# Optimization experiments

Measured on AMD Instinct MI355X. Metric: run time of the kernel, lower is better.

The kernel has to match this reference:

```python
import jax, jax.numpy as jnp
import numpy as np

EMBED = 512
HEADS = 64
DK = EMBED // HEADS  # == n_wires_attn == 8
NW_FFN = 8
FFN = 2048
EPS = 1e-5


def _layernorm(x, g, b):
    mu = jnp.mean(x, axis=-1, keepdims=True)
    var = jnp.var(x, axis=-1, keepdims=True)
    return (x - mu) * jax.lax.rsqrt(var + EPS) * g + b


def setup_inputs() -> dict:
    key = jax.random.key(0)
    ks = jax.random.split(key, 12)
    d = {
        "x": jax.random.normal(ks[0], (4, 1024, EMBED), dtype=jnp.float32),
        # attention quantum RX params (one per wire, shared across heads/tokens)
        "phi": jax.random.normal(ks[1], (DK,), dtype=jnp.float32) * 0.1,
        # combine_heads linear
        "Wc": jax.random.normal(ks[2], (EMBED, EMBED), dtype=jnp.float32) / np.sqrt(EMBED),
        "bc": jnp.zeros((EMBED,), dtype=jnp.float32),
        # FFN quantum RY params
        "theta": jax.random.normal(ks[3], (NW_FFN,), dtype=jnp.float32) * 0.1,
        "W1": jax.random.normal(ks[4], (NW_FFN, FFN), dtype=jnp.float32) / np.sqrt(NW_FFN),
        "b1": jnp.zeros((FFN,), dtype=jnp.float32),
        "W2": jax.random.normal(ks[5], (FFN, EMBED), dtype=jnp.float32) / np.sqrt(FFN),
        "b2": jnp.zeros((EMBED,), dtype=jnp.float32),
        "g1": jnp.ones((EMBED,), dtype=jnp.float32),
        "be1": jnp.zeros((EMBED,), dtype=jnp.float32),
        "g2": jnp.ones((EMBED,), dtype=jnp.float32),
        "be2": jnp.zeros((EMBED,), dtype=jnp.float32),
    }
    return d


def reference(x, phi, Wc, bc, theta, W1, b1, W2, b2, g1, be1, g2, be2):
    B, S, E = x.shape
    # --- quantum attention projections ---
    # Per head-row of DK features: RX(x_i) encoder then trainable RX(phi_i),
    xh = x.reshape(B, S, HEADS, DK)
    qkv = jnp.cos(xh + phi)                     # [B,S,H,DK]
    qkv = jnp.transpose(qkv, (0, 2, 1, 3))      # [B,H,S,DK]
    scores = jnp.einsum('bhqd,bhkd->bhqk', qkv, qkv) / jnp.sqrt(jnp.float32(DK))
    attn = jax.nn.softmax(scores, axis=-1)
    out = jnp.einsum('bhqk,bhkd->bhqd', attn, qkv)
    out = jnp.transpose(out, (0, 2, 1, 3)).reshape(B, S, E)
    attn_out = out @ Wc.T if False else out @ Wc + bc  # combine_heads linear
    x1 = _layernorm(x + attn_out, g1, be1)
    # --- quantum FFN: RX(x_i) then trainable RY(theta_i) -> <Z> = cos(x_i)*cos(theta_i)
    qout = jnp.cos(x1[..., :NW_FFN]) * jnp.cos(theta)   # [B,S,NW_FFN]
    h = jax.nn.relu(qout @ W1 + b1)
    ffn_out = h @ W2 + b2
    return _layernorm(x1 + ffn_out, g2, be2)
```

## Files before the change

### kernel.cpp

```cpp
#include <hip/hip_runtime.h>
#include <hip/hip_bf16.h>
#include <math.h>

#define B 4
#define S 1024
#define E 512
#define H 64
#define DK 8
#define FFN 2048
#define BS (B*S)

#define CSCALE 0.7141879f

#if __has_builtin(__builtin_amdgcn_exp2f)
#define EXP2F(x) __builtin_amdgcn_exp2f(x)
#else
#define EXP2F(x) exp2f(x)
#endif

typedef __attribute__((ext_vector_type(8))) short short8;
typedef __attribute__((ext_vector_type(4))) float float4a;

union U8 { short8 v; unsigned u[4]; };
union F4 { float4a v; float f[4]; };

__device__ __forceinline__ unsigned short f2bf(float f) {
    unsigned u = __builtin_bit_cast(unsigned, f);
    u = (u + 0x7fffu + ((u >> 16) & 1u)) >> 16;
    return (unsigned short)u;
}
__device__ __forceinline__ float bf2f(unsigned short h) {
    return __builtin_bit_cast(float, (unsigned)h << 16);
}
__device__ __forceinline__ unsigned packbf(float a, float b) {
    return __builtin_amdgcn_perm(__builtin_bit_cast(unsigned, a),
                                 __builtin_bit_cast(unsigned, b), 0x07060302u);
}
__device__ __forceinline__ unsigned packbf_rn(float a, float b) {
    return ((unsigned)f2bf(a) << 16) | f2bf(b);
}
__device__ __forceinline__ int pidx(int k) {
    return (k & ~31) | (((k >> 2) & 3) << 3) | (((k >> 4) & 1) << 2) | (k & 3);
}

__global__ __launch_bounds__(512) void attn_conv_kernel(const float* __restrict__ x,
                                                        const float* __restrict__ phi,
                                                        const float* __restrict__ Wc,
                                                        const float* __restrict__ W2,
                                                        const float* __restrict__ W1,
                                                        const float* __restrict__ b1,
                                                        unsigned short* __restrict__ Afrag,
                                                        unsigned short* __restrict__ W2f,
                                                        unsigned short* __restrict__ Wcf,
                                                        unsigned short* __restrict__ W1f) {
    __shared__ unsigned short kv[(S + 16) * DK];
    __shared__ unsigned short vtp[9][S + 8];
    int bid = blockIdx.x;
    int tid = threadIdx.x;

    if (bid >= 512) {
        int idx = (bid - 512) * 512 + tid;
        if (idx < 131072) {
            int lane = idx & 63, c = idx >> 6;
            int ntile = c >> 6, kb32 = c & 63;
            int g = lane >> 4, col = lane & 15;
            int n = ntile * 16 + col, kb = kb32 * 32;
            short8 o;
            #pragma unroll
            for (int j = 0; j < 8; j++) {
                int k = kb + 16 * (j >> 2) + 4 * g + (j & 3);
                o[j] = (short)f2bf(W2[(size_t)k * 512 + n]);
            }
            *(short8*)&W2f[(size_t)idx * 8] = o;
        } else if (idx < 163840) {
            int i2 = idx - 131072;
            int lane = i2 & 63, c = i2 >> 6;
            int ntile = c >> 4, kb32 = c & 15;
            int g = lane >> 4, col = lane & 15;
            int n = ntile * 16 + col, kb = kb32 * 32;
            short8 o;
            #pragma unroll
            for (int j = 0; j < 8; j++)
                o[j] = (short)f2bf(Wc[(size_t)(kb + g * 8 + j) * 512 + n]);
            *(short8*)&Wcf[(size_t)i2 * 8] = o;
        } else {
            int i3 = idx - 163840;
            int lane = i3 & 63, c = i3 >> 6;
            int g = lane >> 4, col = lane & 15;
            int f = (c >> 1) * 32 + (c & 1) * 16 + col;
            short8 o = {0,0,0,0,0,0,0,0};
            if (g == 0) {
                #pragma unroll
                for (int j = 0; j < 8; j++) o[j] = (short)f2bf(W1[j * FFN + f]);
            } else if (g == 1) {
                o[0] = (short)f2bf(b1[f]);
            }
            *(short8*)&W1f[(size_t)i3 * 8] = o;
        }
        return;
    }

    int head = bid >> 1, qhalf = bid & 1;
    int b = head >> 6, hh = head & 63;

    float ph[DK];
    #pragma unroll
    for (int d = 0; d < DK; d++) ph[d] = phi[d];

    const short8 z8 = {0,0,0,0,0,0,0,0};
    for (int r = tid; r < S; r += 512) {
        const float* xp = x + ((size_t)(b * S + r)) * E + hh * DK;
        float4 u = *(const float4*)xp;
        float4 v = *(const float4*)(xp + 4);
        float c[8] = {__cosf(u.x+ph[0]), __cosf(u.y+ph[1]), __cosf(u.z+ph[2]), __cosf(u.w+ph[3]),
                      __cosf(v.x+ph[4]), __cosf(v.y+ph[5]), __cosf(v.z+ph[6]), __cosf(v.w+ph[7])};
        unsigned* kp = (unsigned*)&kv[r * DK];
        #pragma unroll
        for (int d = 0; d < 4; d++)
            kp[d] = packbf_rn(c[2*d+1] * CSCALE, c[2*d] * CSCALE);
        int pr = pidx(r);
        #pragma unroll
        for (int d = 0; d < DK; d++) vtp[d][pr] = f2bf(c[d]);
        vtp[8][pr] = 0x3F80;
    }
    if (tid < 16) *(short8*)&kv[(S + tid) * DK] = z8;
    __syncthreads();

    int w = tid >> 6, lane = tid & 63, col = lane & 15, g = lane >> 4;
    bool g0 = (g == 0);
    int q0 = qhalf * 512 + w * 64;
    const float4a zc = {0.f,0.f,0.f,0.f};

    short8 aq[4];
    #pragma unroll
    for (int t = 0; t < 4; t++)
        aq[t] = g0 ? *(const short8*)&kv[(q0 + t*16 + col) * DK] : z8;

    float4a acc[4];
    #pragma unroll
    for (int t = 0; t < 4; t++) acc[t] = zc;

    int vrow = col < 8 ? col : 8;
    const unsigned short* vbase = &vtp[vrow][0];

    int off0 = g0 ? col * DK : S * DK;
    int off1 = g0 ? (16 + col) * DK : S * DK;
    int stepo = g0 ? 32 * DK : 0;

    for (int kb = 0; kb < S; kb += 32) {
        short8 bk0 = *(const short8*)&kv[off0];
        short8 bk1 = *(const short8*)&kv[off1];
        off0 += stepo; off1 += stepo;
        short8 vf = *(const short8*)(vbase + kb + g * 8);
        #pragma unroll
        for (int t = 0; t < 4; t++) {
            float4a s0 = __builtin_amdgcn_mfma_f32_16x16x32_bf16(bk0, aq[t], zc, 0,0,0);
            float4a s1 = __builtin_amdgcn_mfma_f32_16x16x32_bf16(bk1, aq[t], zc, 0,0,0);
            F4 S0, S1; S0.v = s0; S1.v = s1;
            float e00 = EXP2F(S0.f[0]);
            float e01 = EXP2F(S0.f[1]);
            float e02 = EXP2F(S0.f[2]);
            float e03 = EXP2F(S0.f[3]);
            float e10 = EXP2F(S1.f[0]);
            float e11 = EXP2F(S1.f[1]);
            float e12 = EXP2F(S1.f[2]);
            float e13 = EXP2F(S1.f[3]);
            U8 pf;
            pf.u[0] = packbf(e01, e00);
            pf.u[1] = packbf(e03, e02);
            pf.u[2] = packbf(e11, e10);
            pf.u[3] = packbf(e13, e12);
            acc[t] = __builtin_amdgcn_mfma_f32_16x16x32_bf16(vf, pf.v, acc[t], 0,0,0);
        }
    }
    int lp8 = ((hh & 3) * 16 + col) * 8;
    #pragma unroll
    for (int t = 0; t < 4; t++) {
        F4 a; a.v = acc[t];
        float denom = __shfl(a.f[0], 32 + col);
        float inv = __builtin_amdgcn_rcpf(denom);
        if (g < 2) {
            int chunk = (hh >> 2) * 256 + ((b << 6) | (qhalf << 5) | (w << 2) | t);
            uint2 o;
            o.x = packbf_rn(a.f[1] * inv, a.f[0] * inv);
            o.y = packbf_rn(a.f[3] * inv, a.f[2] * inv);
            *(uint2*)&Afrag[(size_t)chunk * 512 + lp8 + g * 4] = o;
        }
    }
}

__global__ __launch_bounds__(512) void combine_ln1(const unsigned short* __restrict__ Afrag,
                                                   const unsigned short* __restrict__ Wcf,
                                                   const float* __restrict__ bc,
                                                   const float* __restrict__ x,
                                                   const float* __restrict__ g1,
                                                   const float* __restrict__ be1,
                                                   float* __restrict__ x1out,
                                                   unsigned short* __restrict__ qoutbf,
                                                   const float* __restrict__ theta) {
    __shared__ unsigned short As[16 * 64 * 8];
    __shared__ float xout[16][516];
    int tt = blockIdx.x;
    int tid = threadIdx.x;

    for (int i = tid; i < 1024; i += 512)
        *(short8*)&As[i * 8] =
            *(const short8*)&Afrag[((size_t)((i >> 6) * 256 + tt) * 64 + (i & 63)) * 8];
    __syncthreads();

    int w = tid >> 6, lane = tid & 63, col = lane & 15, g = lane >> 4;
    const float4a zc = {0.f,0.f,0.f,0.f};
    float4a acc[4];
    #pragma unroll
    for (int nt = 0; nt < 4; nt++) acc[nt] = zc;

    for (int kb32 = 0; kb32 < 16; kb32++) {
        short8 af = *(const short8*)&As[(kb32 * 64 + lane) * 8];
        #pragma unroll
        for (int nt = 0; nt < 4; nt++) {
            short8 bf = *(const short8*)&Wcf[((size_t)((w * 4 + nt) * 16 + kb32) * 64 + lane) * 8];
            acc[nt] = __builtin_amdgcn_mfma_f32_16x16x32_bf16(af, bf, acc[nt], 0, 0, 0);
        }
    }
    #pragma unroll
    for (int nt = 0; nt < 4; nt++) {
        int n = w * 64 + nt * 16 + col;
        float bb = bc[n];
        #pragma unroll
        for (int r = 0; r < 4; r++)
            xout[g * 4 + r][n] = acc[nt][r] + bb;
    }
    __syncthreads();

    int hl = lane >> 5, l = lane & 31;
    int token = w * 2 + hl;
    int e0 = l * 16;
    size_t grow = ((size_t)tt * 16 + token) * 512;
    float v[16];
    float s = 0.f, sq = 0.f;
    #pragma unroll
    for (int u = 0; u < 4; u++) {
        float4 xv = *(const float4*)&x[grow + e0 + u * 4];
        float4 pv = *(const float4*)&xout[token][e0 + u * 4];
        float a0 = xv.x + pv.x, a1 = xv.y + pv.y, a2 = xv.z + pv.z, a3 = xv.w + pv.w;
        v[u*4] = a0; v[u*4+1] = a1; v[u*4+2] = a2; v[u*4+3] = a3;
        s += a0 + a1 + a2 + a3;
        sq += a0*a0 + a1*a1 + a2*a2 + a3*a3;
    }
    #pragma unroll
    for (int off = 1; off <= 16; off <<= 1) {
        s  += __shfl_xor(s, off);
        sq += __shfl_xor(sq, off);
    }
    float mu = s * (1.f / 512.f);
    float var = sq * (1.f / 512.f) - mu * mu;
    float rstd = rsqrtf(var + 1e-5f);
    float y[16];
    #pragma unroll
    for (int u = 0; u < 4; u++) {
        float4 gv = *(const float4*)&g1[e0 + u * 4];
        float4 bv = *(const float4*)&be1[e0 + u * 4];
        y[u*4]   = (v[u*4]   - mu) * rstd * gv.x + bv.x;
        y[u*4+1] = (v[u*4+1] - mu) * rstd * gv.y + bv.y;
        y[u*4+2] = (v[u*4+2] - mu) * rstd * gv.z + bv.z;
        y[u*4+3] = (v[u*4+3] - mu) * rstd * gv.w + bv.w;
        float4 o = make_float4(y[u*4], y[u*4+1], y[u*4+2], y[u*4+3]);
        *(float4*)&x1out[grow + e0 + u * 4] = o;
    }
    if (l == 0) {
        U8 q;
        q.u[0] = packbf_rn(__cosf(y[1]) * __cosf(theta[1]), __cosf(y[0]) * __cosf(theta[0]));
        q.u[1] = packbf_rn(__cosf(y[3]) * __cosf(theta[3]), __cosf(y[2]) * __cosf(theta[2]));
        q.u[2] = packbf_rn(__cosf(y[5]) * __cosf(theta[5]), __cosf(y[4]) * __cosf(theta[4]));
        q.u[3] = packbf_rn(__cosf(y[7]) * __cosf(theta[7]), __cosf(y[6]) * __cosf(theta[6]));
        *(short8*)&qoutbf[((size_t)tt * 16 + token) * 8] = q.v;
    }
}

__global__ __launch_bounds__(512) void ffn_mfma(const unsigned short* __restrict__ qbf,
                                                const unsigned short* __restrict__ W1fg,
                                                const unsigned short* __restrict__ W2f,
                                                const float* __restrict__ b2,
                                                unsigned short* __restrict__ Cbf) {
    __shared__ unsigned short w1x[FFN * 16];
    int tid = threadIdx.x;
    #pragma unroll
    for (int i = 0; i < 8; i++) {
        int d = tid + i * 512;
        int f = d >> 1, gg = d & 1;
        int kb32 = f >> 5, half = (f >> 4) & 1, fc = f & 15;
        int src = ((kb32 * 2 + half) * 64 + gg * 16 + fc);
        *(short8*)&w1x[f * 16 + gg * 8] = *(const short8*)&W1fg[(size_t)src * 8];
    }
    __syncthreads();

    int w = tid >> 6, lane = tid & 63, col = lane & 15, g = lane >> 4;
    int mw = blockIdx.x * 256 + w * 32;
    int ntile0 = blockIdx.y * 2;
    const short8 z8 = {0,0,0,0,0,0,0,0};
    const short8 one8 = {(short)0x3F80,0,0,0,0,0,0,0};
    const float4a zc = {0.f,0.f,0.f,0.f};

    short8 qf[2];
    #pragma unroll
    for (int t = 0; t < 2; t++)
        qf[t] = (g == 0) ? *(const short8*)&qbf[(size_t)(mw + t * 16 + col) * 8]
                         : (g == 1 ? one8 : z8);

    float4a acc[2][2];
    acc[0][0] = zc; acc[0][1] = zc; acc[1][0] = zc; acc[1][1] = zc;

    const unsigned short* w2p0 = W2f + (size_t)(ntile0 * 64) * 512 + lane * 8;
    const unsigned short* w2p1 = W2f + (size_t)((ntile0 + 1) * 64) * 512 + lane * 8;

    for (int kb32 = 0; kb32 < 64; kb32++) {
        int kb = kb32 * 32;
        short8 w1f0 = (g < 2) ? *(const short8*)&w1x[(kb + col) * 16 + g * 8] : z8;
        short8 w1f1 = (g < 2) ? *(const short8*)&w1x[(kb + 16 + col) * 16 + g * 8] : z8;
        short8 af0 = *(const short8*)(w2p0 + (size_t)kb32 * 512);
        short8 af1 = *(const short8*)(w2p1 + (size_t)kb32 * 512);
        #pragma unroll
        for (int t = 0; t < 2; t++) {
            float4a h0 = __builtin_amdgcn_mfma_f32_16x16x32_bf16(w1f0, qf[t], zc, 0,0,0);
            float4a h1 = __builtin_amdgcn_mfma_f32_16x16x32_bf16(w1f1, qf[t], zc, 0,0,0);
            F4 H0, H1; H0.v = h0; H1.v = h1;
            float e00 = fmaxf(H0.f[0], 0.f);
            float e01 = fmaxf(H0.f[1], 0.f);
            float e02 = fmaxf(H0.f[2], 0.f);
            float e03 = fmaxf(H0.f[3], 0.f);
            float e10 = fmaxf(H1.f[0], 0.f);
            float e11 = fmaxf(H1.f[1], 0.f);
            float e12 = fmaxf(H1.f[2], 0.f);
            float e13 = fmaxf(H1.f[3], 0.f);
            U8 pf;
            pf.u[0] = packbf(e01, e00);
            pf.u[1] = packbf(e03, e02);
            pf.u[2] = packbf(e11, e10);
            pf.u[3] = packbf(e13, e12);
            acc[t][0] = __builtin_amdgcn_mfma_f32_16x16x32_bf16(af0, pf.v, acc[t][0], 0,0,0);
            acc[t][1] = __builtin_amdgcn_mfma_f32_16x16x32_bf16(af1, pf.v, acc[t][1], 0,0,0);
        }
    }
    int n0 = ntile0 * 16;
    #pragma unroll
    for (int nt = 0; nt < 2; nt++) {
        float4 bb = *(const float4*)&b2[n0 + nt * 16 + 4 * g];
        #pragma unroll
        for (int t = 0; t < 2; t++) {
            F4 a; a.v = acc[t][nt];
            uint2 o;
            o.x = packbf_rn(a.f[1] + bb.y, a.f[0] + bb.x);
            o.y = packbf_rn(a.f[3] + bb.w, a.f[2] + bb.z);
            *(uint2*)&Cbf[(size_t)(mw + t * 16 + col) * 512 + n0 + nt * 16 + 4 * g] = o;
        }
    }
}

__global__ __launch_bounds__(256) void ln_kernel(const float* a,
                                                 const unsigned short* __restrict__ r,
                                                 const float* __restrict__ g,
                                                 const float* __restrict__ be,
                                                 float* out) {
    int t = blockIdx.x, tid = threadIdx.x;
    size_t base = (size_t)t * E;
    int e0 = tid * 2;
    float2 av = *(const float2*)&a[base + e0];
    unsigned rv = *(const unsigned*)&r[base + e0];
    float v0 = av.x + bf2f((unsigned short)(rv & 0xffff));
    float v1 = av.y + bf2f((unsigned short)(rv >> 16));
    float s  = v0 + v1;
    float sq = v0 * v0 + v1 * v1;
    #pragma unroll
    for (int off = 32; off > 0; off >>= 1) {
        s  += __shfl_down(s, off);
        sq += __shfl_down(sq, off);
    }
    __shared__ float ls[4], lq[4];
    int wave = tid >> 6, lane = tid & 63;
    if (lane == 0) { ls[wave] = s; lq[wave] = sq; }
    __syncthreads();
    if (tid == 0) {
        float SS = ls[0] + ls[1] + ls[2] + ls[3];
        float QQ = lq[0] + lq[1] + lq[2] + lq[3];
        float mu = SS * (1.f / E);
        float var = QQ * (1.f / E) - mu * mu;
        ls[0] = mu;
        lq[0] = rsqrtf(var + 1e-5f);
    }
    __syncthreads();
    float mu = ls[0], rstd = lq[0];
    float2 gv = *(const float2*)&g[e0];
    float2 bv = *(const float2*)&be[e0];
    float y0 = (v0 - mu) * rstd * gv.x + bv.x;
    float y1 = (v1 - mu) * rstd * gv.y + bv.y;
    *(float2*)&out[base + e0] = make_float2(y0, y1);
}

extern "C" void kernel_launch(void* const* d_in, const int* in_sizes, int n_in,
                              void* d_out, int out_size, void* d_ws, size_t ws_size,
                              hipStream_t stream) {
    const float* x     = (const float*)d_in[0];
    const float* phi   = (const float*)d_in[1];
    const float* Wc    = (const float*)d_in[2];
    const float* bc    = (const float*)d_in[3];
    const float* theta = (const float*)d_in[4];
    const float* W1    = (const float*)d_in[5];
    const float* b1    = (const float*)d_in[6];
    const float* W2    = (const float*)d_in[7];
    const float* b2    = (const float*)d_in[8];
    const float* g1    = (const float*)d_in[9];
    const float* be1   = (const float*)d_in[10];
    const float* g2    = (const float*)d_in[11];
    const float* be2   = (const float*)d_in[12];
    float* out = (float*)d_out;

    float* ws = (float*)d_ws;
    unsigned short* Afrag  = (unsigned short*)ws;
    unsigned short* W2f    = (unsigned short*)(ws + 1048576);
    unsigned short* Wcf    = (unsigned short*)(ws + 1572864);
    unsigned short* W1f    = (unsigned short*)(ws + 1703936);
    unsigned short* qoutbf = (unsigned short*)(ws + 1736704);

    attn_conv_kernel<<<848, 512, 0, stream>>>(x, phi, Wc, W2, W1, b1,
                                              Afrag, W2f, Wcf, W1f);
    combine_ln1<<<256, 512, 0, stream>>>(Afrag, Wcf, bc, x, g1, be1,
                                         out, qoutbf, theta);
    ffn_mfma<<<dim3(16, 16), 512, 0, stream>>>(qoutbf, W1f, W2f, b2, Afrag);
    ln_kernel<<<BS, 256, 0, stream>>>(out, Afrag, g2, be2, out);
}
```

Measured before the change: 164.8 us.

## Fuse FFN GEMM with final layernorm and vectorize attention K/V staging

The FFN MFMA kernel and the separate final layernorm kernel are merged into one kernel. Each block handles 16 tokens across all 512 output columns, keeps the FFN result in fp32 shared memory, and applies the residual add and layernorm in place. This removes one launch and the bf16 round-trip through the workspace. In exchange, each block now streams the entire W2 fragment set from global/L2, with only 256 blocks, where before W1 sat in LDS and W2 tiles were split across a 2D grid. Separately, attention staging now has each thread process 4 consecutive rows so the V-transpose stores become 4-wide vector writes to LDS.

```diff
diff --git a/kernel.cpp b/kernel.cpp
--- a/kernel.cpp
+++ b/kernel.cpp
@@ -19,6 +19,7 @@
 #endif
 
 typedef __attribute__((ext_vector_type(8))) short short8;
+typedef __attribute__((ext_vector_type(4))) short short4v;
 typedef __attribute__((ext_vector_type(4))) float float4a;
 
 union U8 { short8 v; unsigned u[4]; };
@@ -108,20 +109,33 @@
     for (int d = 0; d < DK; d++) ph[d] = phi[d];
 
     const short8 z8 = {0,0,0,0,0,0,0,0};
-    for (int r = tid; r < S; r += 512) {
-        const float* xp = x + ((size_t)(b * S + r)) * E + hh * DK;
-        float4 u = *(const float4*)xp;
-        float4 v = *(const float4*)(xp + 4);
-        float c[8] = {__cosf(u.x+ph[0]), __cosf(u.y+ph[1]), __cosf(u.z+ph[2]), __cosf(u.w+ph[3]),
-                      __cosf(v.x+ph[4]), __cosf(v.y+ph[5]), __cosf(v.z+ph[6]), __cosf(v.w+ph[7])};
-        unsigned* kp = (unsigned*)&kv[r * DK];
-        #pragma unroll
-        for (int d = 0; d < 4; d++)
-            kp[d] = packbf_rn(c[2*d+1] * CSCALE, c[2*d] * CSCALE);
-        int pr = pidx(r);
-        #pragma unroll
-        for (int d = 0; d < DK; d++) vtp[d][pr] = f2bf(c[d]);
-        vtp[8][pr] = 0x3F80;
+    if (tid < 256) {
+        int r4 = tid * 4;
+        unsigned short vb[8][4];
+        #pragma unroll
+        for (int j = 0; j < 4; j++) {
+            const float* xp = x + ((size_t)(b * S + r4 + j)) * E + hh * DK;
+            float4 u = *(const float4*)xp;
+            float4 v = *(const float4*)(xp + 4);
+            float c[8] = {__cosf(u.x+ph[0]), __cosf(u.y+ph[1]), __cosf(u.z+ph[2]), __cosf(u.w+ph[3]),
+                          __cosf(v.x+ph[4]), __cosf(v.y+ph[5]), __cosf(v.z+ph[6]), __cosf(v.w+ph[7])};
+            U8 kr;
+            kr.u[0] = packbf_rn(c[1] * CSCALE, c[0] * CSCALE);
+            kr.u[1] = packbf_rn(c[3] * CSCALE, c[2] * CSCALE);
+            kr.u[2] = packbf_rn(c[5] * CSCALE, c[4] * CSCALE);
+            kr.u[3] = packbf_rn(c[7] * CSCALE, c[6] * CSCALE);
+            *(short8*)&kv[(r4 + j) * DK] = kr.v;
+            #pragma unroll
+            for (int d = 0; d < 8; d++) vb[d][j] = f2bf(c[d]);
+        }
+        int pr = pidx(r4);
+        #pragma unroll
+        for (int d = 0; d < 8; d++) {
+            short4v o = {(short)vb[d][0], (short)vb[d][1], (short)vb[d][2], (short)vb[d][3]};
+            *(short4v*)&vtp[d][pr] = o;
+        }
+        short4v ones = {(short)0x3F80, (short)0x3F80, (short)0x3F80, (short)0x3F80};
+        *(short4v*)&vtp[8][pr] = ones;
     }
     if (tid < 16) *(short8*)&kv[(S + tid) * DK] = z8;
     __syncthreads();
@@ -277,123 +291,97 @@
     }
 }
 
-__global__ __launch_bounds__(512) void ffn_mfma(const unsigned short* __restrict__ qbf,
-                                                const unsigned short* __restrict__ W1fg,
-                                                const unsigned short* __restrict__ W2f,
-                                                const float* __restrict__ b2,
-                                                unsigned short* __restrict__ Cbf) {
-    __shared__ unsigned short w1x[FFN * 16];
+__global__ __launch_bounds__(512) void ffn_ln2(const unsigned short* __restrict__ qbf,
+                                               const unsigned short* __restrict__ W1f,
+                                               const unsigned short* __restrict__ W2f,
+                                               const float* __restrict__ b2,
+                                               const float* __restrict__ g2,
+                                               const float* __restrict__ be2,
+                                               float* out) {
+    __shared__ float xout[16][516];
+    int tt = blockIdx.x;
     int tid = threadIdx.x;
-    #pragma unroll
-    for (int i = 0; i < 8; i++) {
-        int d = tid + i * 512;
-        int f = d >> 1, gg = d & 1;
-        int kb32 = f >> 5, half = (f >> 4) & 1, fc = f & 15;
-        int src = ((kb32 * 2 + half) * 64 + gg * 16 + fc);
-        *(short8*)&w1x[f * 16 + gg * 8] = *(const short8*)&W1fg[(size_t)src * 8];
-    }
-    __syncthreads();
-
     int w = tid >> 6, lane = tid & 63, col = lane & 15, g = lane >> 4;
-    int mw = blockIdx.x * 256 + w * 32;
-    int ntile0 = blockIdx.y * 2;
     const short8 z8 = {0,0,0,0,0,0,0,0};
     const short8 one8 = {(short)0x3F80,0,0,0,0,0,0,0};
     const float4a zc = {0.f,0.f,0.f,0.f};
 
-    short8 qf[2];
-    #pragma unroll
-    for (int t = 0; t < 2; t++)
-        qf[t] = (g == 0) ? *(const short8*)&qbf[(size_t)(mw + t * 16 + col) * 8]
+    short8 qf = (g == 0) ? *(const short8*)&qbf[(size_t)(tt * 16 + col) * 8]
                          : (g == 1 ? one8 : z8);
 
-    float4a acc[2][2];
-    acc[0][0] = zc; acc[0][1] = zc; acc[1][0] = zc; acc[1][1] = zc;
-
-    const unsigned short* w2p0 = W2f + (size_t)(ntile0 * 64) * 512 + lane * 8;
-    const unsigned short* w2p1 = W2f + (size_t)((ntile0 + 1) * 64) * 512 + lane * 8;
-
+    float4a acc[4];
+    #pragma unroll
+    for (int nt = 0; nt < 4; nt++) acc[nt] = zc;
+
+    const unsigned short* w1p = W1f + lane * 8;
     for (int kb32 = 0; kb32 < 64; kb32++) {
-        int kb = kb32 * 32;
-        short8 w1f0 = (g < 2) ? *(const short8*)&w1x[(kb + col) * 16 + g * 8] : z8;
-        short8 w1f1 = (g < 2) ? *(const short8*)&w1x[(kb + 16 + col) * 16 + g * 8] : z8;
-        short8 af0 = *(const short8*)(w2p0 + (size_t)kb32 * 512);
-        short8 af1 = *(const short8*)(w2p1 + (size_t)kb32 * 512);
-        #pragma unroll
-        for (int t = 0; t < 2; t++) {
-            float4a h0 = __builtin_amdgcn_mfma_f32_16x16x32_bf16(w1f0, qf[t], zc, 0,0,0);
-            float4a h1 = __builtin_amdgcn_mfma_f32_16x16x32_bf16(w1f1, qf[t], zc, 0,0,0);
-            F4 H0, H1; H0.v = h0; H1.v = h1;
-            float e00 = fmaxf(H0.f[0], 0.f);
-            float e01 = fmaxf(H0.f[1], 0.f);
-            float e02 = fmaxf(H0.f[2], 0.f);
-            float e03 = fmaxf(H0.f[3], 0.f);
-            float e10 = fmaxf(H1.f[0], 0.f);
-            float e11 = fmaxf(H1.f[1], 0.f);
-            float e12 = fmaxf(H1.f[2], 0.f);
-            float e13 = fmaxf(H1.f[3], 0.f);
-            U8 pf;
-            pf.u[0] = packbf(e01, e00);
-            pf.u[1] = packbf(e03, e02);
-            pf.u[2] = packbf(e11, e10);
-            pf.u[3] = packbf(e13, e12);
-            acc[t][0] = __builtin_amdgcn_mfma_f32_16x16x32_bf16(af0, pf.v, acc[t][0], 0,0,0);
-            acc[t][1] = __builtin_amdgcn_mfma_f32_16x16x32_bf16(af1, pf.v, acc[t][1], 0,0,0);
-        }
-    }
-    int n0 = ntile0 * 16;
-    #pragma unroll
-    for (int nt = 0; nt < 2; nt++) {
-        float4 bb = *(const float4*)&b2[n0 + nt * 16 + 4 * g];
-        #pragma unroll
-        for (int t = 0; t < 2; t++) {
-            F4 a; a.v = acc[t][nt];
-            uint2 o;
-            o.x = packbf_rn(a.f[1] + bb.y, a.f[0] + bb.x);
-            o.y = packbf_rn(a.f[3] + bb.w, a.f[2] + bb.z);
-            *(uint2*)&Cbf[(size_t)(mw + t * 16 + col) * 512 + n0 + nt * 16 + 4 * g] = o;
-        }
-    }
-}
-
-__global__ __launch_bounds__(256) void ln_kernel(const float* a,
-                                                 const unsigned short* __restrict__ r,
-                                                 const float* __restrict__ g,
-                                                 const float* __restrict__ be,
-                                                 float* out) {
-    int t = blockIdx.x, tid = threadIdx.x;
-    size_t base = (size_t)t * E;
-    int e0 = tid * 2;
-    float2 av = *(const float2*)&a[base + e0];
-    unsigned rv = *(const unsigned*)&r[base + e0];
-    float v0 = av.x + bf2f((unsigned short)(rv & 0xffff));
-    float v1 = av.y + bf2f((unsigned short)(rv >> 16));
-    float s  = v0 + v1;
-    float sq = v0 * v0 + v1 * v1;
-    #pragma unroll
-    for (int off = 32; off > 0; off >>= 1) {
-        s  += __shfl_down(s, off);
-        sq += __shfl_down(sq, off);
-    }
-    __shared__ float ls[4], lq[4];
-    int wave = tid >> 6, lane = tid & 63;
-    if (lane == 0) { ls[wave] = s; lq[wave] = sq; }
+        short8 w1f0 = *(const short8*)(w1p + (size_t)(kb32 * 2) * 512);
+        short8 w1f1 = *(const short8*)(w1p + (size_t)(kb32 * 2 + 1) * 512);
+        float4a h0 = __builtin_amdgcn_mfma_f32_16x16x32_bf16(w1f0, qf, zc, 0,0,0);
+        float4a h1 = __builtin_amdgcn_mfma_f32_16x16x32_bf16(w1f1, qf, zc, 0,0,0);
+        F4 H0, H1; H0.v = h0; H1.v = h1;
+        float e00 = fmaxf(H0.f[0], 0.f);
+        float e01 = fmaxf(H0.f[1], 0.f);
+        float e02 = fmaxf(H0.f[2], 0.f);
+        float e03 = fmaxf(H0.f[3], 0.f);
+        float e10 = fmaxf(H1.f[0], 0.f);
+        float e11 = fmaxf(H1.f[1], 0.f);
+        float e12 = fmaxf(H1.f[2], 0.f);
+        float e13 = fmaxf(H1.f[3], 0.f);
+        U8 pf;
+        pf.u[0] = packbf(e01, e00);
+        pf.u[1] = packbf(e03, e02);
+        pf.u[2] = packbf(e11, e10);
+        pf.u[3] = packbf(e13, e12);
+        #pragma unroll
+        for (int nt = 0; nt < 4; nt++) {
+            short8 af = *(const short8*)&W2f[((size_t)((w * 4 + nt) * 64 + kb32) * 64 + lane) * 8];
+            acc[nt] = __builtin_amdgcn_mfma_f32_16x16x32_bf16(af, pf.v, acc[nt], 0,0,0);
+        }
+    }
+    #pragma unroll
+    for (int nt = 0; nt < 4; nt++) {
+        int n = (w * 4 + nt) * 16 + 4 * g;
+        float4 bb = *(const float4*)&b2[n];
+        F4 a; a.v = acc[nt];
+        *(float4*)&xout[col][n] = make_float4(a.f[0] + bb.x, a.f[1] + bb.y,
+                                              a.f[2] + bb.z, a.f[3] + bb.w);
+    }
     __syncthreads();
-    if (tid == 0) {
-        float SS = ls[0] + ls[1] + ls[2] + ls[3];
-        float QQ = lq[0] + lq[1] + lq[2] + lq[3];
-        float mu = SS * (1.f / E);
-        float var = QQ * (1.f / E) - mu * mu;
-        ls[0] = mu;
-        lq[0] = rsqrtf(var + 1e-5f);
-    }
-    __syncthreads();
-    float mu = ls[0], rstd = lq[0];
-    float2 gv = *(const float2*)&g[e0];
-    float2 bv = *(const float2*)&be[e0];
-    float y0 = (v0 - mu) * rstd * gv.x + bv.x;
-    float y1 = (v1 - mu) * rstd * gv.y + bv.y;
-    *(float2*)&out[base + e0] = make_float2(y0, y1);
+
+    int hl = lane >> 5, l = lane & 31;
+    int token = w * 2 + hl;
+    int e0 = l * 16;
+    size_t grow = ((size_t)tt * 16 + token) * 512;
+    float v[16];
+    float s = 0.f, sq = 0.f;
+    #pragma unroll
+    for (int u = 0; u < 4; u++) {
+        float4 xv = *(const float4*)&out[grow + e0 + u * 4];
+        float4 pv = *(const float4*)&xout[token][e0 + u * 4];
+        float a0 = xv.x + pv.x, a1 = xv.y + pv.y, a2 = xv.z + pv.z, a3 = xv.w + pv.w;
+        v[u*4] = a0; v[u*4+1] = a1; v[u*4+2] = a2; v[u*4+3] = a3;
+        s += a0 + a1 + a2 + a3;
+        sq += a0*a0 + a1*a1 + a2*a2 + a3*a3;
+    }
+    #pragma unroll
+    for (int off = 1; off <= 16; off <<= 1) {
+        s  += __shfl_xor(s, off);
+        sq += __shfl_xor(sq, off);
+    }
+    float mu = s * (1.f / 512.f);
+    float var = sq * (1.f / 512.f) - mu * mu;
+    float rstd = rsqrtf(var + 1e-5f);
+    #pragma unroll
+    for (int u = 0; u < 4; u++) {
+        float4 gv = *(const float4*)&g2[e0 + u * 4];
+        float4 bv = *(const float4*)&be2[e0 + u * 4];
+        float4 o = make_float4((v[u*4]   - mu) * rstd * gv.x + bv.x,
+                               (v[u*4+1] - mu) * rstd * gv.y + bv.y,
+                               (v[u*4+2] - mu) * rstd * gv.z + bv.z,
+                               (v[u*4+3] - mu) * rstd * gv.w + bv.w);
+        *(float4*)&out[grow + e0 + u * 4] = o;
+    }
 }
 
 extern "C" void kernel_launch(void* const* d_in, const int* in_sizes, int n_in,
@@ -425,6 +413,5 @@
                                               Afrag, W2f, Wcf, W1f);
     combine_ln1<<<256, 512, 0, stream>>>(Afrag, Wcf, bc, x, g1, be1,
                                          out, qoutbf, theta);
-    ffn_mfma<<<dim3(16, 16), 512, 0, stream>>>(qoutbf, W1f, W2f, b2, Afrag);
-    ln_kernel<<<BS, 256, 0, stream>>>(out, Afrag, g2, be2, out);
-}
+    ffn_ln2<<<256, 512, 0, stream>>>(qoutbf, W1f, W2f, b2, g2, be2, out);
+}
```

Measured after the change: 183.1 us. 1.11x slower.
